# Optimization experiments

Measured on AMD Instinct MI355X. Metric: run time of the kernel, lower is better.

## Reference

```python
import jax, jax.numpy as jnp
import numpy as np

N_NODES = 100000
N_EDGES = 1_600_000


def setup_inputs() -> dict:
    key = jax.random.key(0)
    ks = jax.random.split(key, 18)
    glorot = lambda k, fi, fo: jax.random.normal(k, (fi, fo), jnp.float32) * np.sqrt(2.0 / (fi + fo))
    inp = {
        "x": jax.random.normal(ks[0], (N_NODES, 5), jnp.float32),
        "edge_index": jax.random.randint(ks[1], (2, N_EDGES), 0, N_NODES, jnp.int64 if jax.config.jax_enable_x64 else jnp.int32),
        "W1": glorot(ks[2], 5, 32),  "b1": jnp.zeros((32,), jnp.float32),
        "W2": glorot(ks[3], 32, 32), "b2": jnp.zeros((32,), jnp.float32),
        "W3": glorot(ks[4], 32, 32), "b3": jnp.zeros((32,), jnp.float32),
        "Wd": glorot(ks[5], 32, 1),  "bd": jnp.zeros((1,), jnp.float32),
        "Wa": glorot(ks[6], 32, 1),  "ba": jnp.zeros((1,), jnp.float32),
        "Wt": glorot(ks[7], 32, 2),  "bt": jnp.zeros((2,), jnp.float32),
        "Wact": glorot(ks[8], 32, 9), "bact": jnp.zeros((9,), jnp.float32),
    }
    return inp


def _gcn_layer(x, row, col, norm, W, b):
    # GCNConv(add_self_loops=False): out[col] += norm * (x @ W)[row], then + bias
    h = x @ W                                  # [N, F_out]
    msg = h[row] * norm[:, None]               # [E, F_out]
    return jax.ops.segment_sum(msg, col, num_segments=N_NODES) + b


def reference(x, edge_index, W1, b1, W2, b2, W3, b3, Wd, bd, Wa, ba, Wt, bt, Wact, bact):
    row, col = edge_index[0], edge_index[1]
    # symmetric gcn normalization: deg over targets (unit edge weights)
    deg = jax.ops.segment_sum(jnp.ones((row.shape[0],), x.dtype), col, num_segments=N_NODES)
    dis = jnp.where(deg > 0, jax.lax.rsqrt(jnp.maximum(deg, 1.0)), 0.0)
    norm = dis[row] * dis[col]                 # [E]

    h = jax.nn.relu(_gcn_layer(x, row, col, norm, W1, b1))   # dropout = identity (eval)
    h = jax.nn.relu(_gcn_layer(h, row, col, norm, W2, b2))
    h = jax.nn.relu(_gcn_layer(h, row, col, norm, W3, b3))

    distance_scores = (h @ Wd + bd)[:, 0]      # [N]
    attention_scores = (h @ Wa + ba)[:, 0]     # [N]
    target_idx = jnp.argmax(attention_scores)
    h_t = h[target_idx]                        # [32]
    target_location_score = h_t @ Wt + bt      # [2]
    action_logits = h_t @ Wact + bact          # [9]
    return distance_scores, attention_scores, target_location_score, action_logits
```

## Files before the change

### kernel.cpp

```cpp
#include <hip/hip_runtime.h>
#include <hip/hip_fp16.h>
#include <math.h>

#define N_NODES 100000
#define F 32
#define BUCKET 64
#define NB ((N_NODES + BUCKET - 1) / BUCKET)
#define NBLK 128
#define SMAX 1536

__global__ void hist_kernel(const int* __restrict__ col, int* __restrict__ counts, int E) {
    __shared__ int hist[NB];
    int tid = threadIdx.x, blk = blockIdx.x;
    for (int i = tid; i < NB; i += 256) hist[i] = 0;
    __syncthreads();
    int chunk = (E + NBLK - 1) / NBLK;
    int beg = blk * chunk;
    int end = beg + chunk; if (end > E) end = E;
    for (int e = beg + tid; e < end; e += 256) atomicAdd(&hist[col[e] >> 6], 1);
    __syncthreads();
    for (int i = tid; i < NB; i += 256) counts[(size_t)blk * NB + i] = hist[i];
}

__global__ void tot_kernel(const int* __restrict__ counts, int* __restrict__ tot) {
    int b = blockIdx.x * 256 + threadIdx.x;
    if (b >= NB) return;
    int s = 0;
    for (int blk = 0; blk < NBLK; blk++) s += counts[(size_t)blk * NB + b];
    tot[b] = s;
}

__global__ void offA_kernel(const int* __restrict__ tot, int* __restrict__ bucket_base,
                            int* __restrict__ rowstart) {
    __shared__ int psum[1024];
    int tid = threadIdx.x;
    int b0 = 2 * tid, b1 = 2 * tid + 1;
    int t0 = (b0 < NB) ? tot[b0] : 0;
    int t1 = (b1 < NB) ? tot[b1] : 0;
    int s = t0 + t1;
    psum[tid] = s;
    __syncthreads();
    for (int off = 1; off < 1024; off <<= 1) {
        int v = (tid >= off) ? psum[tid - off] : 0;
        __syncthreads();
        psum[tid] += v;
        __syncthreads();
    }
    int excl = psum[tid] - s;
    if (b0 < NB) bucket_base[b0] = excl;
    if (b1 < NB) bucket_base[b1] = excl + t0;
    if (tid == 1023) { bucket_base[NB] = psum[1023]; rowstart[N_NODES] = psum[1023]; }
}

__global__ void offB_kernel(const int* __restrict__ counts, const int* __restrict__ bucket_base,
                            int* __restrict__ boff) {
    int b = blockIdx.x * 256 + threadIdx.x;
    if (b >= NB) return;
    int running = bucket_base[b];
    for (int blk = 0; blk < NBLK; blk++) {
        boff[(size_t)blk * NB + b] = running;
        running += counts[(size_t)blk * NB + b];
    }
}

__global__ void scatter_kernel(const int* __restrict__ row, const int* __restrict__ col,
                               const int* __restrict__ boff, unsigned* __restrict__ storage, int E) {
    __shared__ int cur[NB];
    int tid = threadIdx.x, blk = blockIdx.x;
    for (int i = tid; i < NB; i += 256) cur[i] = boff[(size_t)blk * NB + i];
    __syncthreads();
    int chunk = (E + NBLK - 1) / NBLK;
    int beg = blk * chunk;
    int end = beg + chunk; if (end > E) end = E;
    for (int e = beg + tid; e < end; e += 256) {
        int c = col[e], r = row[e];
        int pos = atomicAdd(&cur[c >> 6], 1);
        storage[pos] = ((unsigned)(c & 63) << 17) | (unsigned)r;
    }
}

__global__ void csr_build_kernel(const unsigned* __restrict__ storage, const int* __restrict__ bucket_base,
                                 int* __restrict__ rowstart, int* __restrict__ csr_src,
                                 float* __restrict__ dis, const float* __restrict__ x,
                                 float* __restrict__ xd, int n) {
    __shared__ unsigned sh[SMAX];
    __shared__ int outloc[SMAX];
    __shared__ int hist[BUCKET];
    __shared__ int pre[BUCKET];
    __shared__ int cur[BUCKET];
    __shared__ float dloc[BUCKET];
    int b = blockIdx.x, tid = threadIdx.x;
    if (tid < BUCKET) hist[tid] = 0;
    __syncthreads();
    int base = bucket_base[b];
    int tot = bucket_base[b + 1] - base;
    if (tot > SMAX) tot = SMAX;
    for (int i = tid; i < tot; i += 256) sh[i] = storage[base + i];
    __syncthreads();
    for (int i = tid; i < tot; i += 256) atomicAdd(&hist[sh[i] >> 17], 1);
    __syncthreads();
    if (tid < BUCKET) pre[tid] = hist[tid];
    __syncthreads();
    for (int off = 1; off < BUCKET; off <<= 1) {
        int v = 0;
        if (tid < BUCKET && tid >= off) v = pre[tid - off];
        __syncthreads();
        if (tid < BUCKET && tid >= off) pre[tid] += v;
        __syncthreads();
    }
    if (tid < BUCKET) {
        int excl = pre[tid] - hist[tid];
        cur[tid] = excl;
        int node = b * BUCKET + tid;
        if (node < n) {
            rowstart[node] = base + excl;
            int d = hist[tid];
            float dv = (d > 0) ? rsqrtf((float)d) : 0.0f;
            dis[node] = dv;
            dloc[tid] = dv;
        }
    }
    __syncthreads();
    for (int i = tid; i < BUCKET * 8; i += 256) {
        int nl = i >> 3, f = i & 7;
        int node = b * BUCKET + nl;
        if (node < n) xd[(size_t)node * 8 + f] = (f < 5) ? dloc[nl] * x[(size_t)node * 5 + f] : 0.0f;
    }
    for (int i = tid; i < tot; i += 256) {
        unsigned p = sh[i];
        int pos = atomicAdd(&cur[p >> 17], 1);
        outloc[pos] = (int)(p & 0x1FFFF);
    }
    __syncthreads();
    for (int i = tid; i < tot; i += 256) csr_src[base + i] = outloc[i];
}

__global__ void layer1_fused(const float* __restrict__ xd, const int* __restrict__ rowstart,
                             const int* __restrict__ csr_src, const float* __restrict__ dis,
                             const float* __restrict__ W1, const float* __restrict__ b1,
                             __half* __restrict__ gda, int n) {
    __shared__ float Ws[5 * F];
    __shared__ float s1s[32][8];
    int tid = threadIdx.x;
    if (tid < 5 * F) Ws[tid] = W1[tid];
    int grp = tid >> 3, f = tid & 7;
    int node = blockIdx.x * 32 + grp;
    float sum = 0.0f;
    if (node < n) {
        int start = rowstart[node], end = rowstart[node + 1];
        float a0 = 0, a1 = 0, a2 = 0, a3 = 0, a4 = 0, a5 = 0, a6 = 0, a7 = 0;
        int i = start;
        for (; i + 7 < end; i += 8) {
            int r0 = csr_src[i], r1 = csr_src[i+1], r2 = csr_src[i+2], r3 = csr_src[i+3];
            int r4 = csr_src[i+4], r5 = csr_src[i+5], r6 = csr_src[i+6], r7 = csr_src[i+7];
            a0 += xd[r0*8+f]; a1 += xd[r1*8+f]; a2 += xd[r2*8+f]; a3 += xd[r3*8+f];
            a4 += xd[r4*8+f]; a5 += xd[r5*8+f]; a6 += xd[r6*8+f]; a7 += xd[r7*8+f];
        }
        for (; i < end; i++) a0 += xd[csr_src[i]*8+f];
        sum = ((a0+a1)+(a2+a3)) + ((a4+a5)+(a6+a7));
    }
    s1s[grp][f] = sum;
    __syncthreads();
    if (node < n) {
        float dv = dis[node];
        float sk0 = dv * s1s[grp][0], sk1 = dv * s1s[grp][1], sk2 = dv * s1s[grp][2];
        float sk3 = dv * s1s[grp][3], sk4 = dv * s1s[grp][4];
        int fb = f * 4;
#pragma unroll
        for (int j = 0; j < 4; j++) {
            int ff = fb + j;
            float acc = b1[ff] + sk0 * Ws[0*F+ff] + sk1 * Ws[1*F+ff] + sk2 * Ws[2*F+ff]
                       + sk3 * Ws[3*F+ff] + sk4 * Ws[4*F+ff];
            float h = acc > 0.0f ? acc : 0.0f;
            gda[(size_t)node * F + ff] = __float2half(dv * h);
        }
    }
}

__global__ void layer_mid_fused(const __half2* __restrict__ gin, const int* __restrict__ rowstart,
                                const int* __restrict__ csr_src, const float* __restrict__ dis,
                                const float* __restrict__ W, const float* __restrict__ bb,
                                __half2* __restrict__ gout, int n) {
    __shared__ float Ws[F * F];
    __shared__ float hs[16][F + 1];
    int tid = threadIdx.x;
    for (int i = tid; i < F * F; i += 256) Ws[i] = W[i];
    int grp = tid >> 4;
    int l2 = tid & 15;
    int node = blockIdx.x * 16 + grp;
    float dv = 0.0f;
    if (node < n) {
        int start = rowstart[node], end = rowstart[node + 1];
        float accx[4] = {0,0,0,0}, accy[4] = {0,0,0,0};
        int i = start;
        for (; i + 15 < end; i += 16) {
            int r[16];
#pragma unroll
            for (int j = 0; j < 16; j++) r[j] = csr_src[i + j];
            __half2 hv[16];
#pragma unroll
            for (int j = 0; j < 16; j++) hv[j] = gin[(size_t)r[j] * 16 + l2];
#pragma unroll
            for (int j = 0; j < 16; j++) {
                float2 fv = __half22float2(hv[j]);
                accx[j & 3] += fv.x; accy[j & 3] += fv.y;
            }
        }
        for (; i + 7 < end; i += 8) {
            int r[8];
#pragma unroll
            for (int j = 0; j < 8; j++) r[j] = csr_src[i + j];
            __half2 hv[8];
#pragma unroll
            for (int j = 0; j < 8; j++) hv[j] = gin[(size_t)r[j] * 16 + l2];
#pragma unroll
            for (int j = 0; j < 8; j++) {
                float2 fv = __half22float2(hv[j]);
                accx[j & 3] += fv.x; accy[j & 3] += fv.y;
            }
        }
        for (; i < end; i++) {
            float2 fv = __half22float2(gin[(size_t)csr_src[i] * 16 + l2]);
            accx[0] += fv.x; accy[0] += fv.y;
        }
        dv = dis[node];
        hs[grp][2*l2]   = dv * ((accx[0]+accx[1]) + (accx[2]+accx[3]));
        hs[grp][2*l2+1] = dv * ((accy[0]+accy[1]) + (accy[2]+accy[3]));
    }
    __syncthreads();
    if (node < n) {
        int fx = 2*l2, fy = 2*l2+1;
        float accx = bb[fx], accy = bb[fy];
#pragma unroll
        for (int k = 0; k < F; k++) {
            float hv = hs[grp][k];
            accx += hv * Ws[k*F+fx];
            accy += hv * Ws[k*F+fy];
        }
        float hx = accx > 0.0f ? accx : 0.0f;
        float hy = accy > 0.0f ? accy : 0.0f;
        gout[(size_t)node*16 + l2] = __floats2half2_rn(dv * hx, dv * hy);
    }
}

__global__ void layer_last_fused(const __half2* __restrict__ gin, const int* __restrict__ rowstart,
                                 const int* __restrict__ csr_src, const float* __restrict__ dis,
                                 const float* __restrict__ W3, const float* __restrict__ b3,
                                 const float* __restrict__ Wd, const float* __restrict__ bd,
                                 const float* __restrict__ Wa, const float* __restrict__ ba,
                                 float* __restrict__ out, float* __restrict__ pmax,
                                 int* __restrict__ pidx, int n) {
    __shared__ float Ws[F * F];
    __shared__ float hs[16][F + 1];
    __shared__ float gmax[16];
    __shared__ int gidx[16];
    int tid = threadIdx.x;
    for (int i = tid; i < F * F; i += 256) Ws[i] = W3[i];
    int grp = tid >> 4;
    int l2 = tid & 15;
    int node = blockIdx.x * 16 + grp;
    float dv = 0.0f;
    if (node < n) {
        int start = rowstart[node], end = rowstart[node + 1];
        float accx[4] = {0,0,0,0}, accy[4] = {0,0,0,0};
        int i = start;
        for (; i + 15 < end; i += 16) {
            int r[16];
#pragma unroll
            for (int j = 0; j < 16; j++) r[j] = csr_src[i + j];
            __half2 hv[16];
#pragma unroll
            for (int j = 0; j < 16; j++) hv[j] = gin[(size_t)r[j] * 16 + l2];
#pragma unroll
            for (int j = 0; j < 16; j++) {
                float2 fv = __half22float2(hv[j]);
                accx[j & 3] += fv.x; accy[j & 3] += fv.y;
            }
        }
        for (; i + 7 < end; i += 8) {
            int r[8];
#pragma unroll
            for (int j = 0; j < 8; j++) r[j] = csr_src[i + j];
            __half2 hv[8];
#pragma unroll
            for (int j = 0; j < 8; j++) hv[j] = gin[(size_t)r[j] * 16 + l2];
#pragma unroll
            for (int j = 0; j < 8; j++) {
                float2 fv = __half22float2(hv[j]);
                accx[j & 3] += fv.x; accy[j & 3] += fv.y;
            }
        }
        for (; i < end; i++) {
            float2 fv = __half22float2(gin[(size_t)csr_src[i] * 16 + l2]);
            accx[0] += fv.x; accy[0] += fv.y;
        }
        dv = dis[node];
        hs[grp][2*l2]   = dv * ((accx[0]+accx[1]) + (accx[2]+accx[3]));
        hs[grp][2*l2+1] = dv * ((accy[0]+accy[1]) + (accy[2]+accy[3]));
    }
    __syncthreads();
    if (node < n) {
        int fx = 2*l2, fy = 2*l2+1;
        float accx = b3[fx], accy = b3[fy];
#pragma unroll
        for (int k = 0; k < F; k++) {
            float hv = hs[grp][k];
            accx += hv * Ws[k*F+fx];
            accy += hv * Ws[k*F+fy];
        }
        float hx = accx > 0.0f ? accx : 0.0f;
        float hy = accy > 0.0f ? accy : 0.0f;
        float dterm = hx * Wd[fx] + hy * Wd[fy];
        float aterm = hx * Wa[fx] + hy * Wa[fy];
#pragma unroll
        for (int off = 8; off > 0; off >>= 1) {
            dterm += __shfl_xor(dterm, off);
            aterm += __shfl_xor(aterm, off);
        }
        if (l2 == 0) {
            out[node] = dterm + bd[0];
            float asc = aterm + ba[0];
            out[N_NODES + node] = asc;
            gmax[grp] = asc;
            gidx[grp] = node;
        }
    } else if (l2 == 0) {
        gmax[grp] = -INFINITY;
        gidx[grp] = 0x7fffffff;
    }
    __syncthreads();
    if (tid == 0) {
        float best = gmax[0]; int bi = gidx[0];
        for (int g = 1; g < 16; g++) {
            if (gmax[g] > best || (gmax[g] == best && gidx[g] < bi)) { best = gmax[g]; bi = gidx[g]; }
        }
        pmax[blockIdx.x] = best;
        pidx[blockIdx.x] = bi;
    }
}

__global__ void final_kernel(const float* __restrict__ pmax, const int* __restrict__ pidx, int nblocks,
                             const __half* __restrict__ gin, const int* __restrict__ rowstart,
                             const int* __restrict__ csr_src, const float* __restrict__ dis,
                             const float* __restrict__ W3, const float* __restrict__ b3,
                             const float* __restrict__ Wt, const float* __restrict__ bt,
                             const float* __restrict__ Wact, const float* __restrict__ bact,
                             float* __restrict__ out) {
    __shared__ float smax[256];
    __shared__ int sidx[256];
    __shared__ float part[8][F];
    __shared__ float hrow[F];
    __shared__ float ht[F];
    int tid = threadIdx.x;
    float best = -INFINITY; int bi = 0x7fffffff;
    for (int i = tid; i < nblocks; i += 256) {
        float v = pmax[i]; int ix = pidx[i];
        if (v > best || (v == best && ix < bi)) { best = v; bi = ix; }
    }
    smax[tid] = best; sidx[tid] = bi;
    __syncthreads();
    for (int st = 128; st > 0; st >>= 1) {
        if (tid < st) {
            float v2 = smax[tid + st]; int i2 = sidx[tid + st];
            if (v2 > smax[tid] || (v2 == smax[tid] && i2 < sidx[tid])) { smax[tid] = v2; sidx[tid] = i2; }
        }
        __syncthreads();
    }
    int target = sidx[0];
    int g = tid >> 5, f = tid & 31;
    int start = rowstart[target], end = rowstart[target + 1];
    float acc = 0.0f;
    for (int i = start + g; i < end; i += 8)
        acc += __half2float(gin[(size_t)csr_src[i] * F + f]);
    part[g][f] = acc;
    __syncthreads();
    if (tid < F) {
        float s = 0.0f;
#pragma unroll
        for (int gg = 0; gg < 8; gg++) s += part[gg][tid];
        hrow[tid] = dis[target] * s;
    }
    __syncthreads();
    if (tid < F) {
        float a = b3[tid];
#pragma unroll
        for (int k = 0; k < F; k++) a += hrow[k] * W3[k*F+tid];
        ht[tid] = a > 0.0f ? a : 0.0f;
    }
    __syncthreads();
    if (tid < 2) {
        float a = bt[tid];
#pragma unroll
        for (int k = 0; k < F; k++) a += ht[k] * Wt[k*2+tid];
        out[2 * N_NODES + tid] = a;
    } else if (tid < 11) {
        int j = tid - 2;
        float a = bact[j];
#pragma unroll
        for (int k = 0; k < F; k++) a += ht[k] * Wact[k*9+j];
        out[2 * N_NODES + 2 + j] = a;
    }
}

extern "C" void kernel_launch(void* const* d_in, const int* in_sizes, int n_in,
                              void* d_out, int out_size, void* d_ws, size_t ws_size,
                              hipStream_t stream) {
    const float* x  = (const float*)d_in[0];
    const int*   ei = (const int*)d_in[1];
    const int E = in_sizes[1] / 2;
    const int* row = ei;
    const int* col = ei + E;
    const float* W1 = (const float*)d_in[2];
    const float* b1 = (const float*)d_in[3];
    const float* W2 = (const float*)d_in[4];
    const float* b2 = (const float*)d_in[5];
    const float* W3 = (const float*)d_in[6];
    const float* b3 = (const float*)d_in[7];
    const float* Wd = (const float*)d_in[8];
    const float* bd = (const float*)d_in[9];
    const float* Wa = (const float*)d_in[10];
    const float* ba = (const float*)d_in[11];
    const float* Wt = (const float*)d_in[12];
    const float* bt = (const float*)d_in[13];
    const float* Wact = (const float*)d_in[14];
    const float* bact = (const float*)d_in[15];

    float* out = (float*)d_out;
    float* ws  = (float*)d_ws;

    float*    dis      = ws;
    float*    xd       = ws + N_NODES;
    __half*   gd_a     = (__half*)(ws + (size_t)17 * N_NODES);
    __half*   gd_b     = (__half*)(ws + (size_t)33 * N_NODES);
    unsigned* storage  = (unsigned*)(ws + (size_t)33 * N_NODES);
    int*      bucket_base = (int*)(ws + (size_t)49 * N_NODES);
    int*      counts   = bucket_base + NB + 1;
    int*      boff     = counts + NBLK * NB;
    int*      rowstart = boff + NBLK * NB;
    int*      csr_src  = rowstart + N_NODES + 1;
    float*    pmax     = (float*)(csr_src + E);
    int*      pidx     = (int*)(pmax + 12500);
    int*      tot      = pidx + 12500;

    const int B = 256;
    const int nb16 = (N_NODES + 15) / 16;

    hist_kernel<<<NBLK, B, 0, stream>>>(col, counts, E);
    tot_kernel<<<(NB + 255) / 256, B, 0, stream>>>(counts, tot);
    offA_kernel<<<1, 1024, 0, stream>>>(tot, bucket_base, rowstart);
    offB_kernel<<<(NB + 255) / 256, B, 0, stream>>>(counts, bucket_base, boff);
    scatter_kernel<<<NBLK, B, 0, stream>>>(row, col, boff, storage, E);
    csr_build_kernel<<<NB, B, 0, stream>>>(storage, bucket_base, rowstart, csr_src, dis, x, xd, N_NODES);

    layer1_fused<<<(N_NODES + 31) / 32, B, 0, stream>>>(xd, rowstart, csr_src, dis, W1, b1, gd_a, N_NODES);

    layer_mid_fused<<<nb16, B, 0, stream>>>((const __half2*)gd_a, rowstart, csr_src, dis,
                                            W2, b2, (__half2*)gd_b, N_NODES);

    layer_last_fused<<<nb16, B, 0, stream>>>((const __half2*)gd_b, rowstart, csr_src, dis,
                                             W3, b3, Wd, bd, Wa, ba, out, pmax, pidx, N_NODES);
    final_kernel<<<1, B, 0, stream>>>(pmax, pidx, nb16, gd_b, rowstart, csr_src, dis,
                                      W3, b3, Wt, bt, Wact, bact, out);
}
```

Before: 262.7 us.

## Gather neighbor features with 8 lanes per node using 8-byte loads and shuffled indices

The mid and last GCN layers now assign 8 lanes per node instead of 16. Each lane loads a uint2 holding four fp16 features, so a block covers 32 nodes. Neighbor indices are read cooperatively, one per lane, broadcast with shuffles, and the next batch is prefetched, which removes the redundant per-lane index loads. This halves the number of load instructions per gathered row and spreads the index traffic across lanes. In exchange it uses fewer accumulators per lane, and the node<n guards are dropped, which is safe only because N_NODES is divisible by 32.

```diff
diff --git a/kernel.cpp b/kernel.cpp
--- a/kernel.cpp
+++ b/kernel.cpp
@@ -177,161 +177,146 @@
     }
 }
 
-__global__ void layer_mid_fused(const __half2* __restrict__ gin, const int* __restrict__ rowstart,
+__device__ __forceinline__ void gather8lane(const uint2* __restrict__ gin2,
+                                            const int* __restrict__ csr_src,
+                                            int start, int end, int l, int E,
+                                            float& a0, float& a1, float& a2, float& a3) {
+    a0 = a1 = a2 = a3 = 0.0f;
+    int i = start;
+    if (i + 8 <= end) {
+        int safe = i + l; if (safe > E - 1) safe = E - 1;
+        int myidx = csr_src[safe];
+        while (i + 8 <= end) {
+            int nexti = i + 8;
+            int nextidx = 0;
+            if (nexti + 8 <= end) {
+                int s2 = nexti + l; if (s2 > E - 1) s2 = E - 1;
+                nextidx = csr_src[s2];
+            }
+#pragma unroll
+            for (int j = 0; j < 8; j++) {
+                int r = __shfl(myidx, j, 8);
+                uint2 v = gin2[(size_t)r * 8 + l];
+                __half2 h0 = *(__half2*)&v.x;
+                __half2 h1 = *(__half2*)&v.y;
+                float2 f0 = __half22float2(h0);
+                float2 f1 = __half22float2(h1);
+                a0 += f0.x; a1 += f0.y; a2 += f1.x; a3 += f1.y;
+            }
+            myidx = nextidx;
+            i = nexti;
+        }
+    }
+    for (; i < end; i++) {
+        int r = csr_src[i];
+        uint2 v = gin2[(size_t)r * 8 + l];
+        __half2 h0 = *(__half2*)&v.x;
+        __half2 h1 = *(__half2*)&v.y;
+        float2 f0 = __half22float2(h0);
+        float2 f1 = __half22float2(h1);
+        a0 += f0.x; a1 += f0.y; a2 += f1.x; a3 += f1.y;
+    }
+}
+
+__global__ void layer_mid_fused(const uint2* __restrict__ gin2, const int* __restrict__ rowstart,
                                 const int* __restrict__ csr_src, const float* __restrict__ dis,
                                 const float* __restrict__ W, const float* __restrict__ bb,
-                                __half2* __restrict__ gout, int n) {
+                                uint2* __restrict__ gout2, int n, int E) {
     __shared__ float Ws[F * F];
-    __shared__ float hs[16][F + 1];
+    __shared__ float hs[32][F + 1];
     int tid = threadIdx.x;
     for (int i = tid; i < F * F; i += 256) Ws[i] = W[i];
-    int grp = tid >> 4;
-    int l2 = tid & 15;
-    int node = blockIdx.x * 16 + grp;
-    float dv = 0.0f;
-    if (node < n) {
-        int start = rowstart[node], end = rowstart[node + 1];
-        float accx[4] = {0,0,0,0}, accy[4] = {0,0,0,0};
-        int i = start;
-        for (; i + 15 < end; i += 16) {
-            int r[16];
-#pragma unroll
-            for (int j = 0; j < 16; j++) r[j] = csr_src[i + j];
-            __half2 hv[16];
-#pragma unroll
-            for (int j = 0; j < 16; j++) hv[j] = gin[(size_t)r[j] * 16 + l2];
-#pragma unroll
-            for (int j = 0; j < 16; j++) {
-                float2 fv = __half22float2(hv[j]);
-                accx[j & 3] += fv.x; accy[j & 3] += fv.y;
-            }
-        }
-        for (; i + 7 < end; i += 8) {
-            int r[8];
-#pragma unroll
-            for (int j = 0; j < 8; j++) r[j] = csr_src[i + j];
-            __half2 hv[8];
-#pragma unroll
-            for (int j = 0; j < 8; j++) hv[j] = gin[(size_t)r[j] * 16 + l2];
-#pragma unroll
-            for (int j = 0; j < 8; j++) {
-                float2 fv = __half22float2(hv[j]);
-                accx[j & 3] += fv.x; accy[j & 3] += fv.y;
-            }
-        }
-        for (; i < end; i++) {
-            float2 fv = __half22float2(gin[(size_t)csr_src[i] * 16 + l2]);
-            accx[0] += fv.x; accy[0] += fv.y;
-        }
-        dv = dis[node];
-        hs[grp][2*l2]   = dv * ((accx[0]+accx[1]) + (accx[2]+accx[3]));
-        hs[grp][2*l2+1] = dv * ((accy[0]+accy[1]) + (accy[2]+accy[3]));
-    }
-    __syncthreads();
-    if (node < n) {
-        int fx = 2*l2, fy = 2*l2+1;
-        float accx = bb[fx], accy = bb[fy];
-#pragma unroll
-        for (int k = 0; k < F; k++) {
-            float hv = hs[grp][k];
-            accx += hv * Ws[k*F+fx];
-            accy += hv * Ws[k*F+fy];
-        }
-        float hx = accx > 0.0f ? accx : 0.0f;
-        float hy = accy > 0.0f ? accy : 0.0f;
-        gout[(size_t)node*16 + l2] = __floats2half2_rn(dv * hx, dv * hy);
-    }
-}
-
-__global__ void layer_last_fused(const __half2* __restrict__ gin, const int* __restrict__ rowstart,
+    int grp = tid >> 3;
+    int l = tid & 7;
+    int node = blockIdx.x * 32 + grp;
+    int start = rowstart[node], end = rowstart[node + 1];
+    float a0, a1, a2, a3;
+    gather8lane(gin2, csr_src, start, end, l, E, a0, a1, a2, a3);
+    float dv = dis[node];
+    int fb = 4 * l;
+    hs[grp][fb]     = dv * a0;
+    hs[grp][fb + 1] = dv * a1;
+    hs[grp][fb + 2] = dv * a2;
+    hs[grp][fb + 3] = dv * a3;
+    __syncthreads();
+    float acc0 = bb[fb], acc1 = bb[fb+1], acc2 = bb[fb+2], acc3 = bb[fb+3];
+#pragma unroll
+    for (int k = 0; k < F; k++) {
+        float hv = hs[grp][k];
+        acc0 += hv * Ws[k*F+fb];
+        acc1 += hv * Ws[k*F+fb+1];
+        acc2 += hv * Ws[k*F+fb+2];
+        acc3 += hv * Ws[k*F+fb+3];
+    }
+    float h0 = acc0 > 0.0f ? acc0 : 0.0f;
+    float h1 = acc1 > 0.0f ? acc1 : 0.0f;
+    float h2 = acc2 > 0.0f ? acc2 : 0.0f;
+    float h3 = acc3 > 0.0f ? acc3 : 0.0f;
+    __half2 o0 = __floats2half2_rn(dv * h0, dv * h1);
+    __half2 o1 = __floats2half2_rn(dv * h2, dv * h3);
+    uint2 pack;
+    pack.x = *(unsigned*)&o0;
+    pack.y = *(unsigned*)&o1;
+    gout2[(size_t)node * 8 + l] = pack;
+}
+
+__global__ void layer_last_fused(const uint2* __restrict__ gin2, const int* __restrict__ rowstart,
                                  const int* __restrict__ csr_src, const float* __restrict__ dis,
                                  const float* __restrict__ W3, const float* __restrict__ b3,
                                  const float* __restrict__ Wd, const float* __restrict__ bd,
                                  const float* __restrict__ Wa, const float* __restrict__ ba,
                                  float* __restrict__ out, float* __restrict__ pmax,
-                                 int* __restrict__ pidx, int n) {
+                                 int* __restrict__ pidx, int n, int E) {
     __shared__ float Ws[F * F];
-    __shared__ float hs[16][F + 1];
-    __shared__ float gmax[16];
-    __shared__ int gidx[16];
+    __shared__ float hs[32][F + 1];
+    __shared__ float gmax[32];
+    __shared__ int gidx[32];
     int tid = threadIdx.x;
     for (int i = tid; i < F * F; i += 256) Ws[i] = W3[i];
-    int grp = tid >> 4;
-    int l2 = tid & 15;
-    int node = blockIdx.x * 16 + grp;
-    float dv = 0.0f;
-    if (node < n) {
-        int start = rowstart[node], end = rowstart[node + 1];
-        float accx[4] = {0,0,0,0}, accy[4] = {0,0,0,0};
-        int i = start;
-        for (; i + 15 < end; i += 16) {
-            int r[16];
-#pragma unroll
-            for (int j = 0; j < 16; j++) r[j] = csr_src[i + j];
-            __half2 hv[16];
-#pragma unroll
-            for (int j = 0; j < 16; j++) hv[j] = gin[(size_t)r[j] * 16 + l2];
-#pragma unroll
-            for (int j = 0; j < 16; j++) {
-                float2 fv = __half22float2(hv[j]);
-                accx[j & 3] += fv.x; accy[j & 3] += fv.y;
-            }
-        }
-        for (; i + 7 < end; i += 8) {
-            int r[8];
-#pragma unroll
-            for (int j = 0; j < 8; j++) r[j] = csr_src[i + j];
-            __half2 hv[8];
-#pragma unroll
-            for (int j = 0; j < 8; j++) hv[j] = gin[(size_t)r[j] * 16 + l2];
-#pragma unroll
-            for (int j = 0; j < 8; j++) {
-                float2 fv = __half22float2(hv[j]);
-                accx[j & 3] += fv.x; accy[j & 3] += fv.y;
-            }
-        }
-        for (; i < end; i++) {
-            float2 fv = __half22float2(gin[(size_t)csr_src[i] * 16 + l2]);
-            accx[0] += fv.x; accy[0] += fv.y;
-        }
-        dv = dis[node];
-        hs[grp][2*l2]   = dv * ((accx[0]+accx[1]) + (accx[2]+accx[3]));
-        hs[grp][2*l2+1] = dv * ((accy[0]+accy[1]) + (accy[2]+accy[3]));
-    }
-    __syncthreads();
-    if (node < n) {
-        int fx = 2*l2, fy = 2*l2+1;
-        float accx = b3[fx], accy = b3[fy];
-#pragma unroll
-        for (int k = 0; k < F; k++) {
-            float hv = hs[grp][k];
-            accx += hv * Ws[k*F+fx];
-            accy += hv * Ws[k*F+fy];
-        }
-        float hx = accx > 0.0f ? accx : 0.0f;
-        float hy = accy > 0.0f ? accy : 0.0f;
-        float dterm = hx * Wd[fx] + hy * Wd[fy];
-        float aterm = hx * Wa[fx] + hy * Wa[fy];
-#pragma unroll
-        for (int off = 8; off > 0; off >>= 1) {
-            dterm += __shfl_xor(dterm, off);
-            aterm += __shfl_xor(aterm, off);
-        }
-        if (l2 == 0) {
-            out[node] = dterm + bd[0];
-            float asc = aterm + ba[0];
-            out[N_NODES + node] = asc;
-            gmax[grp] = asc;
-            gidx[grp] = node;
-        }
-    } else if (l2 == 0) {
-        gmax[grp] = -INFINITY;
-        gidx[grp] = 0x7fffffff;
+    int grp = tid >> 3;
+    int l = tid & 7;
+    int node = blockIdx.x * 32 + grp;
+    int start = rowstart[node], end = rowstart[node + 1];
+    float a0, a1, a2, a3;
+    gather8lane(gin2, csr_src, start, end, l, E, a0, a1, a2, a3);
+    float dv = dis[node];
+    int fb = 4 * l;
+    hs[grp][fb]     = dv * a0;
+    hs[grp][fb + 1] = dv * a1;
+    hs[grp][fb + 2] = dv * a2;
+    hs[grp][fb + 3] = dv * a3;
+    __syncthreads();
+    float acc0 = b3[fb], acc1 = b3[fb+1], acc2 = b3[fb+2], acc3 = b3[fb+3];
+#pragma unroll
+    for (int k = 0; k < F; k++) {
+        float hv = hs[grp][k];
+        acc0 += hv * Ws[k*F+fb];
+        acc1 += hv * Ws[k*F+fb+1];
+        acc2 += hv * Ws[k*F+fb+2];
+        acc3 += hv * Ws[k*F+fb+3];
+    }
+    float h0 = acc0 > 0.0f ? acc0 : 0.0f;
+    float h1 = acc1 > 0.0f ? acc1 : 0.0f;
+    float h2 = acc2 > 0.0f ? acc2 : 0.0f;
+    float h3 = acc3 > 0.0f ? acc3 : 0.0f;
+    float dterm = h0 * Wd[fb] + h1 * Wd[fb+1] + h2 * Wd[fb+2] + h3 * Wd[fb+3];
+    float aterm = h0 * Wa[fb] + h1 * Wa[fb+1] + h2 * Wa[fb+2] + h3 * Wa[fb+3];
+#pragma unroll
+    for (int off = 4; off > 0; off >>= 1) {
+        dterm += __shfl_xor(dterm, off, 8);
+        aterm += __shfl_xor(aterm, off, 8);
+    }
+    if (l == 0) {
+        out[node] = dterm + bd[0];
+        float asc = aterm + ba[0];
+        out[N_NODES + node] = asc;
+        gmax[grp] = asc;
+        gidx[grp] = node;
     }
     __syncthreads();
     if (tid == 0) {
         float best = gmax[0]; int bi = gidx[0];
-        for (int g = 1; g < 16; g++) {
+        for (int g = 1; g < 32; g++) {
             if (gmax[g] > best || (gmax[g] == best && gidx[g] < bi)) { best = gmax[g]; bi = gidx[g]; }
         }
         pmax[blockIdx.x] = best;
@@ -443,7 +428,7 @@
     int*      tot      = pidx + 12500;
 
     const int B = 256;
-    const int nb16 = (N_NODES + 15) / 16;
+    const int nb32 = (N_NODES + 31) / 32;
 
     hist_kernel<<<NBLK, B, 0, stream>>>(col, counts, E);
     tot_kernel<<<(NB + 255) / 256, B, 0, stream>>>(counts, tot);
@@ -452,13 +437,13 @@
     scatter_kernel<<<NBLK, B, 0, stream>>>(row, col, boff, storage, E);
     csr_build_kernel<<<NB, B, 0, stream>>>(storage, bucket_base, rowstart, csr_src, dis, x, xd, N_NODES);
 
-    layer1_fused<<<(N_NODES + 31) / 32, B, 0, stream>>>(xd, rowstart, csr_src, dis, W1, b1, gd_a, N_NODES);
-
-    layer_mid_fused<<<nb16, B, 0, stream>>>((const __half2*)gd_a, rowstart, csr_src, dis,
-                                            W2, b2, (__half2*)gd_b, N_NODES);
-
-    layer_last_fused<<<nb16, B, 0, stream>>>((const __half2*)gd_b, rowstart, csr_src, dis,
-                                             W3, b3, Wd, bd, Wa, ba, out, pmax, pidx, N_NODES);
-    final_kernel<<<1, B, 0, stream>>>(pmax, pidx, nb16, gd_b, rowstart, csr_src, dis,
+    layer1_fused<<<nb32, B, 0, stream>>>(xd, rowstart, csr_src, dis, W1, b1, gd_a, N_NODES);
+
+    layer_mid_fused<<<nb32, B, 0, stream>>>((const uint2*)gd_a, rowstart, csr_src, dis,
+                                            W2, b2, (uint2*)gd_b, N_NODES, E);
+
+    layer_last_fused<<<nb32, B, 0, stream>>>((const uint2*)gd_b, rowstart, csr_src, dis,
+                                             W3, b3, Wd, bd, Wa, ba, out, pmax, pidx, N_NODES, E);
+    final_kernel<<<1, B, 0, stream>>>(pmax, pidx, nb32, gd_b, rowstart, csr_src, dis,
                                       W3, b3, Wt, bt, Wact, bact, out);
 }
```

Result: faster. 239.3 us (-8.9%).
